# Performance work log

Hardware: AMD Instinct MI355X
Metric: run time of the kernel (lower is better)

## Reference

```python
import jax, jax.numpy as jnp
import numpy as np

B, S, D, H = 2, 2048, 1024, 16
DH = D // H

def setup_inputs() -> dict:
    key = jax.random.key(0)
    ks = jax.random.split(key, 6)
    scale = 0.02
    return {
        "x":  jax.random.normal(ks[0], (B, S, D), jnp.float32),
        "Wq": jax.random.normal(ks[1], (D, D), jnp.float32) * scale,
        "Wk": jax.random.normal(ks[2], (D, D), jnp.float32) * scale,
        "Wv": jax.random.normal(ks[3], (D, D), jnp.float32) * scale,
        "Wo": jax.random.normal(ks[4], (D, D), jnp.float32) * scale,
        "bo": jnp.zeros((D,), jnp.float32),
    }

def reference(x, Wq, Wk, Wv, Wo, bo):
    b, s, d = x.shape
    h, dh = H, DH
    # projections -> [b, h, s, dh]
    def split_heads(t):
        return t.reshape(b, s, h, dh).transpose(0, 2, 1, 3)
    q = split_heads(x @ Wq)
    k = split_heads(x @ Wk)
    v = split_heads(x @ Wv)
    # scaled causal attention
    scores = jnp.einsum('bhqd,bhkd->bhqk', q, k) / jnp.sqrt(jnp.float32(dh))
    causal = jnp.tril(jnp.ones((s, s), bool))
    scores = jnp.where(causal[None, None], scores, -jnp.inf)
    attn = jax.nn.softmax(scores, axis=-1)
    # dropout p=0.0 -> identity
    ctx = jnp.einsum('bhqk,bhkd->bhqd', attn, v)
    ctx = ctx.transpose(0, 2, 1, 3).reshape(b, s, d)
    return ctx @ Wo + bo
```

## Files before the change

### kernel.cpp

```cpp
#include <hip/hip_runtime.h>


typedef _Float16 f16;
typedef _Float16 f16x8 __attribute__((ext_vector_type(8)));
typedef _Float16 f16x4 __attribute__((ext_vector_type(4)));
typedef float    f32x4 __attribute__((ext_vector_type(4)));

__device__ __forceinline__ void gload16(const void* g, void* l) {
  __builtin_amdgcn_global_load_lds(
      (const __attribute__((address_space(1))) void*)g,
      (__attribute__((address_space(3))) void*)l, 16, 0, 0);
}

__global__ void cvt_x(const float* __restrict__ x, f16* __restrict__ xb) {
  int idx = blockIdx.x * 256 + threadIdx.x;
  float4 v = ((const float4*)x)[idx];
  f16x4 o = { (f16)v.x, (f16)v.y, (f16)v.z, (f16)v.w };
  ((f16x4*)xb)[idx] = o;
}

__global__ void cvt_w(const float* __restrict__ W0, const float* __restrict__ W1,
                      const float* __restrict__ W2, const float* __restrict__ W3,
                      f16* __restrict__ T0, f16* __restrict__ T1,
                      f16* __restrict__ T2, f16* __restrict__ T3) {
  const float* W = blockIdx.z == 0 ? W0 : blockIdx.z == 1 ? W1 : blockIdx.z == 2 ? W2 : W3;
  f16*        Tt = blockIdx.z == 0 ? T0 : blockIdx.z == 1 ? T1 : blockIdx.z == 2 ? T2 : T3;
  __shared__ f16 tile[64][65];
  int tid = threadIdx.x;
  int k0 = blockIdx.y * 64, n0 = blockIdx.x * 64;
  int rr = tid >> 4, cc = (tid & 15) * 4;
#pragma unroll
  for (int p = 0; p < 4; ++p) {
    int r = rr + p * 16;
    float4 v = *(const float4*)(W + (size_t)(k0 + r) * 1024 + n0 + cc);
    tile[r][cc + 0] = (f16)v.x; tile[r][cc + 1] = (f16)v.y;
    tile[r][cc + 2] = (f16)v.z; tile[r][cc + 3] = (f16)v.w;
  }
  __syncthreads();
#pragma unroll
  for (int p = 0; p < 4; ++p) {
    int r = rr + p * 16;
    f16x4 v;
#pragma unroll
    for (int j = 0; j < 4; ++j) v[j] = tile[cc + j][r];
    *(f16x4*)(Tt + (size_t)(n0 + r) * 1024 + k0 + cc) = v;
  }
}

template <int MODE>
__global__ __launch_bounds__(256, 2)
void gemm_k(const f16* __restrict__ A, const f16* __restrict__ Bt,
            f16* __restrict__ oQ, f16* __restrict__ oK, f16* __restrict__ oV,
            float* __restrict__ oO, const float* __restrict__ bias) {
  constexpr int Kd = 1024;
  __shared__ f16 smem[2 * 128 * 64];
  f16* sA = smem;
  f16* sB = smem + 128 * 64;
  const int tid = threadIdx.x;
  const int lane = tid & 63, wid = tid >> 6;
  const int wr = wid >> 1, wc = wid & 1;
  const int bm = blockIdx.y * 128, bn = blockIdx.x * 128;

  f32x4 acc[4][4] = {};

  for (int k0 = 0; k0 < Kd; k0 += 64) {
#pragma unroll
    for (int p = 0; p < 4; ++p) {
      int c = p * 256 + tid;
      int row = c >> 3;
      int gc = (c & 7) ^ (row & 7);
      gload16(A + (size_t)(bm + row) * Kd + k0 + gc * 8, sA + c * 8);
      gload16(Bt + (size_t)(bn + row) * Kd + k0 + gc * 8, sB + c * 8);
    }
    __syncthreads();
#pragma unroll
    for (int ks = 0; ks < 2; ++ks) {
      f16x8 af[4], bf[4];
#pragma unroll
      for (int m = 0; m < 4; ++m) {
        int row = wr * 64 + m * 16 + (lane & 15);
        int j = (ks * 4 + (lane >> 4)) ^ (row & 7);
        af[m] = *(const f16x8*)((const char*)sA + row * 128 + j * 16);
      }
#pragma unroll
      for (int n = 0; n < 4; ++n) {
        int row = wc * 64 + n * 16 + (lane & 15);
        int j = (ks * 4 + (lane >> 4)) ^ (row & 7);
        bf[n] = *(const f16x8*)((const char*)sB + row * 128 + j * 16);
      }
#pragma unroll
      for (int m = 0; m < 4; ++m)
#pragma unroll
        for (int n = 0; n < 4; ++n)
          acc[m][n] = __builtin_amdgcn_mfma_f32_16x16x32_f16(af[m], bf[n], acc[m][n], 0, 0, 0);
    }
    __syncthreads();
  }

  if constexpr (MODE == 2) {
#pragma unroll
    for (int m = 0; m < 4; ++m) {
      int rbase = bm + wr * 64 + m * 16 + ((lane >> 4) << 2);
#pragma unroll
      for (int n = 0; n < 4; ++n) {
        int ncol = bn + wc * 64 + n * 16 + (lane & 15);
        float bv = bias[ncol];
#pragma unroll
        for (int i = 0; i < 4; ++i)
          oO[(size_t)(rbase + i) * 1024 + ncol] = acc[m][n][i] + bv;
      }
    }
  } else {
    const int seg = bn >> 10;
    if (seg < 2) {
      f16* dst = seg == 0 ? oQ : oK;
#pragma unroll
      for (int m = 0; m < 4; ++m) {
        int rbase = bm + wr * 64 + m * 16 + ((lane >> 4) << 2);
#pragma unroll
        for (int n = 0; n < 4; ++n) {
          int ncol = (bn & 1023) + wc * 64 + n * 16 + (lane & 15);
          int h = ncol >> 6, dh = ncol & 63;
#pragma unroll
          for (int i = 0; i < 4; ++i) {
            int rr = rbase + i;
            int b = rr >> 11, s = rr & 2047;
            dst[(((size_t)(b * 16 + h) * 2048 + s) << 6) + dh] = (f16)acc[m][n][i];
          }
        }
      }
    } else {
      f16* T64 = smem;
      int b = bm >> 11, sbase = bm & 2047;
      int bnl = bn & 1023;
#pragma unroll
      for (int p = 0; p < 2; ++p) {
        if (wr == p) {
#pragma unroll
          for (int m = 0; m < 4; ++m)
#pragma unroll
            for (int n = 0; n < 4; ++n)
#pragma unroll
              for (int i = 0; i < 4; ++i) {
                int rl = m * 16 + ((lane >> 4) << 2) + i;
                int col = wc * 64 + n * 16 + (lane & 15);
                T64[rl * 132 + col] = (f16)acc[m][n][i];
              }
        }
        __syncthreads();
#pragma unroll
        for (int it = 0; it < 4; ++it) {
          int oc = it * 256 + tid;
          int ocol = oc >> 3;
          int och = oc & 7;
          f16x8 v;
#pragma unroll
          for (int j = 0; j < 8; ++j) v[j] = T64[(och * 8 + j) * 132 + ocol];
          int ncol = bnl + ocol;
          int h = ncol >> 6, dh = ncol & 63;
          *(f16x8*)(oV + ((size_t)((b * 16 + h) * 64 + dh) << 11) + sbase + p * 64 + och * 8) = v;
        }
        __syncthreads();
      }
    }
  }
}

__global__ __launch_bounds__(256, 3)
void attn_k(const f16* __restrict__ Q, const f16* __restrict__ Kg,
            const f16* __restrict__ Vt, f16* __restrict__ ctx) {
  __shared__ f16 sK[64 * 64];
  __shared__ f16 sV[64 * 64];
  __shared__ f16 sP[4][16 * 64];
  const int tid = threadIdx.x, lane = tid & 63, wid = tid >> 6;
  const int bh = blockIdx.y;
  const int b = bh >> 4, h = bh & 15;
  const f16* Qb = Q + ((size_t)bh << 17);
  const f16* Kb = Kg + ((size_t)bh << 17);
  const f16* Vb = Vt + ((size_t)bh << 17);

  for (int half = 0; half < 2; ++half) {
    const int qt = half == 0 ? blockIdx.x : 31 - blockIdx.x;

    const int qrow_a = qt * 64 + wid * 16 + (lane & 15);
    f16x8 qf[2];
    qf[0] = *(const f16x8*)(Qb + (size_t)qrow_a * 64 + ((lane >> 4) << 3));
    qf[1] = *(const f16x8*)(Qb + (size_t)qrow_a * 64 + 32 + ((lane >> 4) << 3));

    f32x4 acc[4] = {};
    float m_run[4], l_run[4];
#pragma unroll
    for (int i = 0; i < 4; ++i) { m_run[i] = -INFINITY; l_run[i] = 0.f; }
    const int qg_base = qt * 64 + wid * 16 + ((lane >> 4) << 2);
    const int qmax_w = qt * 64 + wid * 16 + 15;

    for (int kt = 0; kt <= qt; ++kt) {
#pragma unroll
      for (int p = 0; p < 2; ++p) {
        int c = p * 256 + tid;
        int row = c >> 3;
        int gc = (c & 7) ^ (row & 7);
        gload16(Kb + (size_t)(kt * 64 + row) * 64 + gc * 8, sK + c * 8);
        gload16(Vb + (size_t)row * 2048 + kt * 64 + gc * 8, sV + c * 8);
      }
      __syncthreads();

      f32x4 sf[4];
#pragma unroll
      for (int kc = 0; kc < 4; ++kc) {
        if (kt * 64 + kc * 16 <= qmax_w) {
          f32x4 z = {};
#pragma unroll
          for (int ks = 0; ks < 2; ++ks) {
            int row = kc * 16 + (lane & 15);
            int j = (ks * 4 + (lane >> 4)) ^ (row & 7);
            f16x8 kf = *(const f16x8*)((const char*)sK + row * 128 + j * 16);
            z = __builtin_amdgcn_mfma_f32_16x16x32_f16(qf[ks], kf, z, 0, 0, 0);
          }
          sf[kc] = z;
        } else {
          sf[kc] = (f32x4){-1e30f, -1e30f, -1e30f, -1e30f};
        }
      }
#pragma unroll
      for (int kc = 0; kc < 4; ++kc)
#pragma unroll
        for (int i = 0; i < 4; ++i) {
          float s = sf[kc][i] * 0.125f;
          int kg = kt * 64 + kc * 16 + (lane & 15);
          if (kg > qg_base + i) s = -1e30f;
          sf[kc][i] = s;
        }
      float mnew[4], scl[4];
#pragma unroll
      for (int i = 0; i < 4; ++i) {
        float v = fmaxf(fmaxf(sf[0][i], sf[1][i]), fmaxf(sf[2][i], sf[3][i]));
        v = fmaxf(v, __shfl_xor(v, 1));
        v = fmaxf(v, __shfl_xor(v, 2));
        v = fmaxf(v, __shfl_xor(v, 4));
        v = fmaxf(v, __shfl_xor(v, 8));
        float mn = fmaxf(m_run[i], v);
        mnew[i] = mn;
        scl[i] = __expf(m_run[i] - mn);
        m_run[i] = mn;
      }
#pragma unroll
      for (int i = 0; i < 4; ++i) {
        float ls = 0.f;
#pragma unroll
        for (int kc = 0; kc < 4; ++kc) {
          float p = __expf(sf[kc][i] - mnew[i]);
          sf[kc][i] = p;
          ls += p;
        }
        ls += __shfl_xor(ls, 1);
        ls += __shfl_xor(ls, 2);
        ls += __shfl_xor(ls, 4);
        ls += __shfl_xor(ls, 8);
        l_run[i] = l_run[i] * scl[i] + ls;
#pragma unroll
        for (int d = 0; d < 4; ++d) acc[d][i] *= scl[i];
      }
      char* Pw = (char*)(sP[wid]);
#pragma unroll
      for (int kc = 0; kc < 4; ++kc)
#pragma unroll
        for (int i = 0; i < 4; ++i) {
          int row = ((lane >> 4) << 2) + i;
          int col = kc * 16 + (lane & 15);
          int ch = col >> 3;
          *(f16*)(Pw + row * 128 + ((ch ^ (row & 7)) << 4) + ((col & 7) << 1)) = (f16)sf[kc][i];
        }
#pragma unroll
      for (int kk = 0; kk < 2; ++kk) {
        if (kt * 64 + kk * 32 <= qmax_w) {
          int prow = lane & 15;
          int pj = (kk * 4 + (lane >> 4)) ^ (prow & 7);
          f16x8 pa = *(const f16x8*)(Pw + prow * 128 + pj * 16);
#pragma unroll
          for (int d = 0; d < 4; ++d) {
            int vrow = d * 16 + (lane & 15);
            int vj = (kk * 4 + (lane >> 4)) ^ (vrow & 7);
            f16x8 vf = *(const f16x8*)((const char*)sV + vrow * 128 + vj * 16);
            acc[d] = __builtin_amdgcn_mfma_f32_16x16x32_f16(pa, vf, acc[d], 0, 0, 0);
          }
        }
      }
      __syncthreads();
    }
#pragma unroll
    for (int d = 0; d < 4; ++d)
#pragma unroll
      for (int i = 0; i < 4; ++i) {
        int s = qt * 64 + wid * 16 + ((lane >> 4) << 2) + i;
        float val = acc[d][i] / l_run[i];
        ctx[((size_t)(b * 2048 + s) << 10) + (h << 6) + (d << 4) + (lane & 15)] = (f16)val;
      }
  }
}

extern "C" void kernel_launch(void* const* d_in, const int* in_sizes, int n_in,
                              void* d_out, int out_size, void* d_ws, size_t ws_size,
                              hipStream_t stream) {
  const float* x  = (const float*)d_in[0];
  const float* Wq = (const float*)d_in[1];
  const float* Wk = (const float*)d_in[2];
  const float* Wv = (const float*)d_in[3];
  const float* Wo = (const float*)d_in[4];
  const float* bo = (const float*)d_in[5];
  char* ws = (char*)d_ws;
  f16* xb   = (f16*)(ws);
  f16* Wcat = (f16*)(ws + ((size_t)8  << 20));
  f16* Wot  = (f16*)(ws + ((size_t)14 << 20));
  f16* Qb   = (f16*)(ws + ((size_t)16 << 20));
  f16* Kb   = (f16*)(ws + ((size_t)24 << 20));
  f16* Vtb  = (f16*)(ws + ((size_t)32 << 20));
  f16* ctx  = (f16*)(ws + ((size_t)40 << 20));
  const size_t MM = (size_t)1024 * 1024;

  hipLaunchKernelGGL(cvt_x, dim3(4096), dim3(256), 0, stream, x, xb);
  hipLaunchKernelGGL(cvt_w, dim3(16, 16, 4), dim3(256), 0, stream,
                     Wq, Wk, Wv, Wo, Wcat, Wcat + MM, Wcat + 2 * MM, Wot);
  hipLaunchKernelGGL((gemm_k<0>), dim3(24, 32), dim3(256), 0, stream,
                     xb, Wcat, Qb, Kb, Vtb, nullptr, nullptr);
  hipLaunchKernelGGL(attn_k, dim3(16, 32), dim3(256), 0, stream, Qb, Kb, Vtb, ctx);
  hipLaunchKernelGGL((gemm_k<2>), dim3(8, 32), dim3(256), 0, stream,
                     ctx, Wot, nullptr, nullptr, nullptr, (float*)d_out, bo);
}
```

Before: 215.5 us.

## Transpose QK^T MFMA so each lane owns one query row in softmax

```diff
diff --git a/kernel.cpp b/kernel.cpp
--- a/kernel.cpp
+++ b/kernel.cpp
@@ -166,7 +166,7 @@
   }
 }
 
-__global__ __launch_bounds__(256, 3)
+__global__ __launch_bounds__(256, 2)
 void attn_k(const f16* __restrict__ Q, const f16* __restrict__ Kg,
             const f16* __restrict__ Vt, f16* __restrict__ ctx) {
   __shared__ f16 sK[64 * 64];
@@ -178,21 +178,21 @@
   const f16* Qb = Q + ((size_t)bh << 17);
   const f16* Kb = Kg + ((size_t)bh << 17);
   const f16* Vb = Vt + ((size_t)bh << 17);
+  const float SC = 0.1803368801f;
 
   for (int half = 0; half < 2; ++half) {
     const int qt = half == 0 ? blockIdx.x : 31 - blockIdx.x;
-
-    const int qrow_a = qt * 64 + wid * 16 + (lane & 15);
+    const int qbase = qt * 64 + wid * 16;
+    const int qg = qbase + (lane & 15);
+    const int qmax_w = qbase + 15;
+
+    const int qrow_a = qbase + (lane & 15);
     f16x8 qf[2];
     qf[0] = *(const f16x8*)(Qb + (size_t)qrow_a * 64 + ((lane >> 4) << 3));
     qf[1] = *(const f16x8*)(Qb + (size_t)qrow_a * 64 + 32 + ((lane >> 4) << 3));
 
     f32x4 acc[4] = {};
-    float m_run[4], l_run[4];
-#pragma unroll
-    for (int i = 0; i < 4; ++i) { m_run[i] = -INFINITY; l_run[i] = 0.f; }
-    const int qg_base = qt * 64 + wid * 16 + ((lane >> 4) << 2);
-    const int qmax_w = qt * 64 + wid * 16 + 15;
+    float m_run = -INFINITY, l_run = 0.f;
 
     for (int kt = 0; kt <= qt; ++kt) {
 #pragma unroll
@@ -215,7 +215,7 @@
             int row = kc * 16 + (lane & 15);
             int j = (ks * 4 + (lane >> 4)) ^ (row & 7);
             f16x8 kf = *(const f16x8*)((const char*)sK + row * 128 + j * 16);
-            z = __builtin_amdgcn_mfma_f32_16x16x32_f16(qf[ks], kf, z, 0, 0, 0);
+            z = __builtin_amdgcn_mfma_f32_16x16x32_f16(kf, qf[ks], z, 0, 0, 0);
           }
           sf[kc] = z;
         } else {
@@ -223,54 +223,54 @@
         }
       }
 #pragma unroll
+      for (int kc = 0; kc < 4; ++kc) {
+        if (kt * 64 + kc * 16 + 15 > qbase) {
+#pragma unroll
+          for (int i = 0; i < 4; ++i) {
+            int kg = kt * 64 + kc * 16 + ((lane >> 4) << 2) + i;
+            sf[kc][i] = (kg <= qg) ? sf[kc][i] * SC : -1e30f;
+          }
+        } else {
+#pragma unroll
+          for (int i = 0; i < 4; ++i) sf[kc][i] *= SC;
+        }
+      }
+      float v01 = fmaxf(fmaxf(sf[0][0], sf[0][1]), fmaxf(sf[0][2], sf[0][3]));
+      float v23 = fmaxf(fmaxf(sf[1][0], sf[1][1]), fmaxf(sf[1][2], sf[1][3]));
+      float v45 = fmaxf(fmaxf(sf[2][0], sf[2][1]), fmaxf(sf[2][2], sf[2][3]));
+      float v67 = fmaxf(fmaxf(sf[3][0], sf[3][1]), fmaxf(sf[3][2], sf[3][3]));
+      float v = fmaxf(fmaxf(v01, v23), fmaxf(v45, v67));
+      v = fmaxf(v, __shfl_xor(v, 16));
+      v = fmaxf(v, __shfl_xor(v, 32));
+      float mn = fmaxf(m_run, v);
+      float scl = __builtin_amdgcn_exp2f(m_run - mn);
+      m_run = mn;
+      float ls = 0.f;
+#pragma unroll
       for (int kc = 0; kc < 4; ++kc)
 #pragma unroll
         for (int i = 0; i < 4; ++i) {
-          float s = sf[kc][i] * 0.125f;
-          int kg = kt * 64 + kc * 16 + (lane & 15);
-          if (kg > qg_base + i) s = -1e30f;
-          sf[kc][i] = s;
-        }
-      float mnew[4], scl[4];
-#pragma unroll
-      for (int i = 0; i < 4; ++i) {
-        float v = fmaxf(fmaxf(sf[0][i], sf[1][i]), fmaxf(sf[2][i], sf[3][i]));
-        v = fmaxf(v, __shfl_xor(v, 1));
-        v = fmaxf(v, __shfl_xor(v, 2));
-        v = fmaxf(v, __shfl_xor(v, 4));
-        v = fmaxf(v, __shfl_xor(v, 8));
-        float mn = fmaxf(m_run[i], v);
-        mnew[i] = mn;
-        scl[i] = __expf(m_run[i] - mn);
-        m_run[i] = mn;
-      }
-#pragma unroll
-      for (int i = 0; i < 4; ++i) {
-        float ls = 0.f;
-#pragma unroll
-        for (int kc = 0; kc < 4; ++kc) {
-          float p = __expf(sf[kc][i] - mnew[i]);
+          float p = __builtin_amdgcn_exp2f(sf[kc][i] - mn);
           sf[kc][i] = p;
           ls += p;
         }
-        ls += __shfl_xor(ls, 1);
-        ls += __shfl_xor(ls, 2);
-        ls += __shfl_xor(ls, 4);
-        ls += __shfl_xor(ls, 8);
-        l_run[i] = l_run[i] * scl[i] + ls;
-#pragma unroll
-        for (int d = 0; d < 4; ++d) acc[d][i] *= scl[i];
+      ls += __shfl_xor(ls, 16);
+      ls += __shfl_xor(ls, 32);
+      l_run = l_run * scl + ls;
+#pragma unroll
+      for (int i = 0; i < 4; ++i) {
+        float sb = __shfl(scl, ((lane >> 4) << 2) + i);
+#pragma unroll
+        for (int d = 0; d < 4; ++d) acc[d][i] *= sb;
       }
       char* Pw = (char*)(sP[wid]);
 #pragma unroll
-      for (int kc = 0; kc < 4; ++kc)
-#pragma unroll
-        for (int i = 0; i < 4; ++i) {
-          int row = ((lane >> 4) << 2) + i;
-          int col = kc * 16 + (lane & 15);
-          int ch = col >> 3;
-          *(f16*)(Pw + row * 128 + ((ch ^ (row & 7)) << 4) + ((col & 7) << 1)) = (f16)sf[kc][i];
-        }
+      for (int kc = 0; kc < 4; ++kc) {
+        int kbase = kc * 16 + ((lane >> 4) << 2);
+        int ch = kbase >> 3;
+        f16x4 pv = { (f16)sf[kc][0], (f16)sf[kc][1], (f16)sf[kc][2], (f16)sf[kc][3] };
+        *(f16x4*)(Pw + (lane & 15) * 128 + ((ch ^ (lane & 7)) << 4) + ((kbase & 7) << 1)) = pv;
+      }
 #pragma unroll
       for (int kk = 0; kk < 2; ++kk) {
         if (kt * 64 + kk * 32 <= qmax_w) {
@@ -289,13 +289,16 @@
       __syncthreads();
     }
 #pragma unroll
-    for (int d = 0; d < 4; ++d)
-#pragma unroll
-      for (int i = 0; i < 4; ++i) {
-        int s = qt * 64 + wid * 16 + ((lane >> 4) << 2) + i;
-        float val = acc[d][i] / l_run[i];
+    for (int i = 0; i < 4; ++i) {
+      float lb = __shfl(l_run, ((lane >> 4) << 2) + i);
+      float r = 1.f / lb;
+      int s = qbase + ((lane >> 4) << 2) + i;
+#pragma unroll
+      for (int d = 0; d < 4; ++d) {
+        float val = acc[d][i] * r;
         ctx[((size_t)(b * 2048 + s) << 10) + (h << 6) + (d << 4) + (lane & 15)] = (f16)val;
       }
+    }
   }
 }
 
```

Measured after the change: 201.6 us. 1.07x faster.
